# Optimization experiments

Hardware: AMD Instinct MI355X
Metric: run time of the kernel (lower is better)

The kernel has to match this reference:

```python
import jax, jax.numpy as jnp
import numpy as np
from jax import lax

KH, KW, PAD = 3, 3, 1  # kernel_size and paddings from init_kwargs


def _sign_pm1(v):
    # tf.sign with zeros mapped to -1
    return jnp.where(v > 0, jnp.float32(1.0), jnp.float32(-1.0)).astype(v.dtype)


def setup_inputs() -> dict:
    key = jax.random.key(0)
    k1, k2, k3 = jax.random.split(key, 3)
    x = jax.random.normal(k1, (32, 56, 56, 256), dtype=jnp.float32)
    kernel = jax.random.normal(k2, (KH, KW, 256, 256), dtype=jnp.float32) * 0.05
    bias = jax.random.normal(k3, (256,), dtype=jnp.float32) * 0.01
    return {"x": x, "kernel": kernel, "bias": bias}


def reference(x, kernel, bias):
    # pad input spatially (NHWC)
    xp = jnp.pad(x, ((0, 0), (PAD, PAD), (PAD, PAD), (0, 0)))

    # binarize kernel: static batch dim known -> alpha = mean(|W|) over (kh, kw, cin)
    bin_k = _sign_pm1(kernel)
    alpha = jnp.mean(jnp.abs(kernel), axis=(0, 1, 2))  # (Cout,)

    # binarize input: batch dim dynamic in TF -> beta = mean(|x|) over channels, keepdims
    bin_x = _sign_pm1(xp)                               # (N, H+2P, W+2P, C)
    beta = jnp.mean(jnp.abs(xp), axis=3, keepdims=True)  # (N, H+2P, W+2P, 1)

    # K = avg_pool(beta, kernel window, stride 1, VALID)
    K = lax.reduce_window(beta, jnp.float32(0.0), lax.add,
                          (1, KH, KW, 1), (1, 1, 1, 1), 'VALID') / (KH * KW)
    Ka = K * alpha  # (N, H, W, Cout) via broadcast

    conv = lax.conv_general_dilated(
        bin_x, bin_k, window_strides=(1, 1), padding='VALID',
        dimension_numbers=('NHWC', 'HWIO', 'NHWC'))  # (N, H, W, Cout)

    return conv * Ka + bias
```

## Files before the change

kernel.cpp:

```cpp
#include <hip/hip_runtime.h>
#include <cstdint>

#define N_ 32
#define H_ 56
#define W_ 56
#define C_ 256
#define HP 58
#define WP 58


__global__ __launch_bounds__(256) void pack_w(const float* __restrict__ k,
                                              uint64_t* __restrict__ kb,
                                              float* __restrict__ palpha) {
    int idx = blockIdx.x;
    int p = idx >> 2, j = idx & 3;
    int co = threadIdx.x;
    uint64_t bits = 0;
    float s = 0.f;
    #pragma unroll
    for (int b = 0; b < 64; ++b) {
        float v = k[(p * 256 + 4 * b + j) * 256 + co];
        bits |= (uint64_t)(v > 0.f) << b;
        s += fabsf(v);
    }
    kb[((size_t)p * 256 + co) * 4 + j] = bits;
    palpha[idx * 256 + co] = s;
}

__global__ __launch_bounds__(256) void pack_x(const float4* __restrict__ x4,
                                              uint64_t* __restrict__ xb,
                                              float* __restrict__ beta) {
    int bi = blockIdx.x;
    int n = bi / HP, y = bi % HP;
    int wave = threadIdx.x >> 6, lane = threadIdx.x & 63;
    for (int xc = wave; xc < WP; xc += 4) {
        bool inb = (y >= 1 && y <= H_ && xc >= 1 && xc <= W_);
        float4 v = make_float4(0.f, 0.f, 0.f, 0.f);
        if (inb)
            v = x4[(((size_t)n * H_ + (y - 1)) * W_ + (xc - 1)) * 64 + lane];
        uint64_t m0 = __ballot(v.x > 0.f);
        uint64_t m1 = __ballot(v.y > 0.f);
        uint64_t m2 = __ballot(v.z > 0.f);
        uint64_t m3 = __ballot(v.w > 0.f);
        float s = fabsf(v.x) + fabsf(v.y) + fabsf(v.z) + fabsf(v.w);
        #pragma unroll
        for (int m = 32; m >= 1; m >>= 1) s += __shfl_xor(s, m, 64);
        size_t pix = (size_t)bi * WP + xc;
        if (lane < 4) {
            uint64_t mw = (lane == 0) ? m0 : (lane == 1) ? m1 : (lane == 2) ? m2 : m3;
            xb[pix * 4 + lane] = mw;
        }
        if (lane == 0) beta[pix] = s * (1.f / 256.f);
    }
}

__global__ __launch_bounds__(256, 4) void bconv(
        const uint64_t* __restrict__ xb, const float* __restrict__ beta,
        const uint64_t* __restrict__ kb, const float* __restrict__ palpha,
        const float* __restrict__ bias, float* __restrict__ out) {
    int bi = blockIdx.x;
    int n = bi / H_, h = bi % H_;
    int tid = threadIdx.x;
    int half = tid >> 7;
    int col = tid & 127;
    int co = (blockIdx.y << 7) | col;

    __shared__ __align__(16) uint64_t xs[3 * WP * 4];
    __shared__ float brow[3 * WP];
    __shared__ float bS[W_];
    __shared__ uint32_t pb[128 * 15];

    const uint64_t* xsrc = xb + (size_t)(n * HP + h) * WP * 4;
    for (int i = tid; i < 3 * WP * 2; i += 256)
        ((ulonglong2*)xs)[i] = ((const ulonglong2*)xsrc)[i];
    const float* bsrc = beta + (size_t)(n * HP + h) * WP;
    for (int i = tid; i < 3 * WP; i += 256) brow[i] = bsrc[i];
    __syncthreads();

    if (tid < W_) {
        float s = 0.f;
        #pragma unroll
        for (int r = 0; r < 3; ++r)
            #pragma unroll
            for (int d = 0; d < 3; ++d) s += brow[r * WP + tid + d];
        bS[tid] = s * (1.f / 9.f);
    }

    uint64_t kr0[9], kr1[9];
    #pragma unroll
    for (int t = 0; t < 9; ++t) {
        ulonglong2 kp = ((const ulonglong2*)kb)[((size_t)t * 256 + co) * 2 + half];
        kr0[t] = kp.x;
        kr1[t] = kp.y;
    }
    float asum = 0.f;
    #pragma unroll
    for (int i = 0; i < 36; ++i) asum += palpha[i * 256 + co];
    float alpha = asum * (1.f / 2304.f);
    float bv = bias[co];

    for (int chunk = 0; chunk < 4; ++chunk) {
        int w0 = chunk * 14;
        uint32_t acc[14];
        #pragma unroll
        for (int i = 0; i < 14; ++i) acc[i] = 0;

        const uint64_t* base = &xs[w0 * 4 + 2 * half];
        #pragma unroll
        for (int xi = 0; xi < 16; ++xi) {
            #pragma unroll
            for (int r = 0; r < 3; ++r) {
                uint64_t x0 = base[(r * WP + xi) * 4];
                uint64_t x1 = base[(r * WP + xi) * 4 + 1];
                #pragma unroll
                for (int kw = 0; kw < 3; ++kw) {
                    int wl = xi - kw;
                    if (wl >= 0 && wl < 14) {
                        int t = r * 3 + kw;
                        acc[wl] += __popcll(x0 ^ kr0[t]) + __popcll(x1 ^ kr1[t]);
                    }
                }
            }
        }

        __syncthreads();
        if (half == 1) {
            #pragma unroll
            for (int i = 0; i < 14; ++i) pb[col * 15 + i] = acc[i];
        }
        __syncthreads();
        if (half == 0) {
            #pragma unroll
            for (int i = 0; i < 14; ++i) {
                int w = w0 + i;
                int tot = (int)(acc[i] + pb[col * 15 + i]);
                float conv = (float)(2304 - 2 * tot);
                out[((size_t)bi * W_ + w) * C_ + co] = conv * bS[w] * alpha + bv;
            }
        }
    }
}

extern "C" void kernel_launch(void* const* d_in, const int* in_sizes, int n_in,
                              void* d_out, int out_size, void* d_ws, size_t ws_size,
                              hipStream_t stream) {
    const float* x    = (const float*)d_in[0];
    const float* k    = (const float*)d_in[1];
    const float* bias = (const float*)d_in[2];
    float* out = (float*)d_out;

    char* ws = (char*)d_ws;
    uint64_t* kb     = (uint64_t*)(ws);
    float*    palpha = (float*)(ws + 73728);
    uint64_t* xb     = (uint64_t*)(ws + 110592);
    float*    beta   = (float*)(ws + 3555328);

    pack_w<<<36, 256, 0, stream>>>(k, kb, palpha);
    pack_x<<<N_ * HP, 256, 0, stream>>>((const float4*)x, xb, beta);
    bconv<<<dim3(N_ * H_, 2), 256, 0, stream>>>(xb, beta, kb, palpha, bias, out);
}
```

Before: 296.6 us.

## Rewrite binary conv to map output columns to lanes with wave-uniform weights

The convolution kernel is restructured so that each lane owns an input column and loops over 64 output channels per wave. Weight words are read as wave-uniform loads from a new co-major layout, and the three horizontal taps are combined with lane shuffles. Outputs are staged through shared memory for coalesced stores. The weight packing is also split across 1024 threads, alpha gets its own small kernel, and pack_x runs one wave per interior pixel with the padding handled by a memset. The intent is to drop the shared-memory x tile, the two-half reduction and the per-block alpha sums, at the cost of a serial 64-channel loop and extra launches.

New measurement: 427.4 us. 1.44x slower.

```diff
diff --git a/kernel.cpp b/kernel.cpp
--- a/kernel.cpp
+++ b/kernel.cpp
@@ -8,134 +8,130 @@
 #define HP 58
 #define WP 58
 
+#define OFF_KB     0
+#define OFF_PAL    73728
+#define OFF_ALF    110592
+#define OFF_XB     114688
+#define OFF_BETA   3559424
 
-__global__ __launch_bounds__(256) void pack_w(const float* __restrict__ k,
-                                              uint64_t* __restrict__ kb,
-                                              float* __restrict__ palpha) {
-    int idx = blockIdx.x;
-    int p = idx >> 2, j = idx & 3;
-    int co = threadIdx.x;
-    uint64_t bits = 0;
-    float s = 0.f;
+
+__global__ __launch_bounds__(1024) void pack_w(const float* __restrict__ k,
+                                               uint64_t* __restrict__ kb,
+                                               float* __restrict__ palpha) {
+    int p = blockIdx.x >> 2, j = blockIdx.x & 3;
+    int q = threadIdx.x >> 8;
+    int co = threadIdx.x & 255;
+    uint64_t bits = 0; float s = 0.f;
     #pragma unroll
-    for (int b = 0; b < 64; ++b) {
+    for (int i = 0; i < 16; ++i) {
+        int b = q * 16 + i;
         float v = k[(p * 256 + 4 * b + j) * 256 + co];
         bits |= (uint64_t)(v > 0.f) << b;
         s += fabsf(v);
     }
-    kb[((size_t)p * 256 + co) * 4 + j] = bits;
-    palpha[idx * 256 + co] = s;
+    __shared__ uint64_t pb[4][256];
+    __shared__ float ps[4][256];
+    pb[q][co] = bits; ps[q][co] = s;
+    __syncthreads();
+    if (q == 0) {
+        uint64_t w = pb[0][co] | pb[1][co] | pb[2][co] | pb[3][co];
+        float t = ps[0][co] + ps[1][co] + ps[2][co] + ps[3][co];
+        kb[((size_t)co * 9 + p) * 4 + j] = w;
+        palpha[(p * 4 + j) * 256 + co] = t;
+    }
+}
+
+__global__ __launch_bounds__(256) void alpha_k(const float* __restrict__ palpha,
+                                               float* __restrict__ alphaF) {
+    int co = threadIdx.x;
+    float s = 0.f;
+    #pragma unroll
+    for (int i = 0; i < 36; ++i) s += palpha[i * 256 + co];
+    alphaF[co] = s * (1.f / 2304.f);
 }
 
 __global__ __launch_bounds__(256) void pack_x(const float4* __restrict__ x4,
                                               uint64_t* __restrict__ xb,
                                               float* __restrict__ beta) {
-    int bi = blockIdx.x;
-    int n = bi / HP, y = bi % HP;
     int wave = threadIdx.x >> 6, lane = threadIdx.x & 63;
-    for (int xc = wave; xc < WP; xc += 4) {
-        bool inb = (y >= 1 && y <= H_ && xc >= 1 && xc <= W_);
-        float4 v = make_float4(0.f, 0.f, 0.f, 0.f);
-        if (inb)
-            v = x4[(((size_t)n * H_ + (y - 1)) * W_ + (xc - 1)) * 64 + lane];
-        uint64_t m0 = __ballot(v.x > 0.f);
-        uint64_t m1 = __ballot(v.y > 0.f);
-        uint64_t m2 = __ballot(v.z > 0.f);
-        uint64_t m3 = __ballot(v.w > 0.f);
-        float s = fabsf(v.x) + fabsf(v.y) + fabsf(v.z) + fabsf(v.w);
-        #pragma unroll
-        for (int m = 32; m >= 1; m >>= 1) s += __shfl_xor(s, m, 64);
-        size_t pix = (size_t)bi * WP + xc;
-        if (lane < 4) {
-            uint64_t mw = (lane == 0) ? m0 : (lane == 1) ? m1 : (lane == 2) ? m2 : m3;
-            xb[pix * 4 + lane] = mw;
-        }
-        if (lane == 0) beta[pix] = s * (1.f / 256.f);
+    int P = blockIdx.x * 4 + wave;
+    float4 v = x4[(size_t)P * 64 + lane];
+    uint64_t m0 = __ballot(v.x > 0.f);
+    uint64_t m1 = __ballot(v.y > 0.f);
+    uint64_t m2 = __ballot(v.z > 0.f);
+    uint64_t m3 = __ballot(v.w > 0.f);
+    float s = fabsf(v.x) + fabsf(v.y) + fabsf(v.z) + fabsf(v.w);
+    #pragma unroll
+    for (int m = 32; m >= 1; m >>= 1) s += __shfl_xor(s, m, 64);
+    int n = P / (H_ * W_);
+    int r = P % (H_ * W_);
+    int hy = r / W_, wx = r % W_;
+    size_t pp = ((size_t)n * HP + hy + 1) * WP + (wx + 1);
+    if (lane < 4) {
+        uint64_t mw = (lane == 0) ? m0 : (lane == 1) ? m1 : (lane == 2) ? m2 : m3;
+        xb[pp * 4 + lane] = mw;
     }
+    if (lane == 0) beta[pp] = s * (1.f / 256.f);
 }
 
-__global__ __launch_bounds__(256, 4) void bconv(
+__global__ __launch_bounds__(256) void bconv(
         const uint64_t* __restrict__ xb, const float* __restrict__ beta,
-        const uint64_t* __restrict__ kb, const float* __restrict__ palpha,
+        const uint64_t* __restrict__ kb, const float* __restrict__ alphaF,
         const float* __restrict__ bias, float* __restrict__ out) {
-    int bi = blockIdx.x;
-    int n = bi / H_, h = bi % H_;
-    int tid = threadIdx.x;
-    int half = tid >> 7;
-    int col = tid & 127;
-    int co = (blockIdx.y << 7) | col;
+    int bx = blockIdx.x;
+    int n = bx / H_, h = bx % H_;
+    int wave = threadIdx.x >> 6, lane = threadIdx.x & 63;
+    int co0 = wave * 64;
+    int c = lane < 57 ? lane : 57;
 
-    __shared__ __align__(16) uint64_t xs[3 * WP * 4];
-    __shared__ float brow[3 * WP];
-    __shared__ float bS[W_];
-    __shared__ uint32_t pb[128 * 15];
+    uint64_t xw[3][4];
+    #pragma unroll
+    for (int r = 0; r < 3; ++r) {
+        const ulonglong2* p2 =
+            (const ulonglong2*)(xb + ((size_t)(n * HP + h + r) * WP + c) * 4);
+        ulonglong2 a = p2[0], b = p2[1];
+        xw[r][0] = a.x; xw[r][1] = a.y; xw[r][2] = b.x; xw[r][3] = b.y;
+    }
 
-    const uint64_t* xsrc = xb + (size_t)(n * HP + h) * WP * 4;
-    for (int i = tid; i < 3 * WP * 2; i += 256)
-        ((ulonglong2*)xs)[i] = ((const ulonglong2*)xsrc)[i];
-    const float* bsrc = beta + (size_t)(n * HP + h) * WP;
-    for (int i = tid; i < 3 * WP; i += 256) brow[i] = bsrc[i];
-    __syncthreads();
-
-    if (tid < W_) {
-        float s = 0.f;
+    float bSw = 0.f;
+    if (lane < W_) {
         #pragma unroll
         for (int r = 0; r < 3; ++r)
             #pragma unroll
-            for (int d = 0; d < 3; ++d) s += brow[r * WP + tid + d];
-        bS[tid] = s * (1.f / 9.f);
+            for (int d = 0; d < 3; ++d)
+                bSw += beta[(size_t)(n * HP + h + r) * WP + lane + d];
+        bSw *= (1.f / 9.f);
     }
 
-    uint64_t kr0[9], kr1[9];
-    #pragma unroll
-    for (int t = 0; t < 9; ++t) {
-        ulonglong2 kp = ((const ulonglong2*)kb)[((size_t)t * 256 + co) * 2 + half];
-        kr0[t] = kp.x;
-        kr1[t] = kp.y;
-    }
-    float asum = 0.f;
-    #pragma unroll
-    for (int i = 0; i < 36; ++i) asum += palpha[i * 256 + co];
-    float alpha = asum * (1.f / 2304.f);
-    float bv = bias[co];
+    __shared__ float ts[4][W_ * 17];
+    float* t = ts[wave];
+    float* orow = out + (size_t)bx * W_ * C_;
 
-    for (int chunk = 0; chunk < 4; ++chunk) {
-        int w0 = chunk * 14;
-        uint32_t acc[14];
+    for (int ci = 0; ci < 64; ++ci) {
+        int co = co0 + ci;
+        const uint64_t* kr = kb + (size_t)co * 36;
+        uint32_t T0 = 0, T1 = 0, T2 = 0;
         #pragma unroll
-        for (int i = 0; i < 14; ++i) acc[i] = 0;
-
-        const uint64_t* base = &xs[w0 * 4 + 2 * half];
-        #pragma unroll
-        for (int xi = 0; xi < 16; ++xi) {
+        for (int r = 0; r < 3; ++r) {
             #pragma unroll
-            for (int r = 0; r < 3; ++r) {
-                uint64_t x0 = base[(r * WP + xi) * 4];
-                uint64_t x1 = base[(r * WP + xi) * 4 + 1];
-                #pragma unroll
-                for (int kw = 0; kw < 3; ++kw) {
-                    int wl = xi - kw;
-                    if (wl >= 0 && wl < 14) {
-                        int t = r * 3 + kw;
-                        acc[wl] += __popcll(x0 ^ kr0[t]) + __popcll(x1 ^ kr1[t]);
-                    }
-                }
+            for (int j = 0; j < 4; ++j) {
+                uint64_t xv = xw[r][j];
+                T0 += __popcll(xv ^ kr[(r * 3 + 0) * 4 + j]);
+                T1 += __popcll(xv ^ kr[(r * 3 + 1) * 4 + j]);
+                T2 += __popcll(xv ^ kr[(r * 3 + 2) * 4 + j]);
             }
         }
-
-        __syncthreads();
-        if (half == 1) {
-            #pragma unroll
-            for (int i = 0; i < 14; ++i) pb[col * 15 + i] = acc[i];
-        }
-        __syncthreads();
-        if (half == 0) {
+        uint32_t tot = T0 + __shfl_down(T1, 1) + __shfl_down(T2, 2);
+        float conv = (float)(2304 - 2 * (int)tot);
+        float res = conv * bSw * alphaF[co] + bias[co];
+        if (lane < W_) t[lane * 17 + (ci & 15)] = res;
+        if ((ci & 15) == 15) {
+            int cb = co0 + (ci & ~15);
             #pragma unroll
             for (int i = 0; i < 14; ++i) {
-                int w = w0 + i;
-                int tot = (int)(acc[i] + pb[col * 15 + i]);
-                float conv = (float)(2304 - 2 * tot);
-                out[((size_t)bi * W_ + w) * C_ + co] = conv * bS[w] * alpha + bv;
+                int idx = i * 64 + lane;
+                int w = idx >> 4, cc = idx & 15;
+                orow[(size_t)w * C_ + cb + cc] = t[w * 17 + cc];
             }
         }
     }
@@ -150,12 +146,16 @@
     float* out = (float*)d_out;
 
     char* ws = (char*)d_ws;
-    uint64_t* kb     = (uint64_t*)(ws);
-    float*    palpha = (float*)(ws + 73728);
-    uint64_t* xb     = (uint64_t*)(ws + 110592);
-    float*    beta   = (float*)(ws + 3555328);
+    uint64_t* kb     = (uint64_t*)(ws + OFF_KB);
+    float*    palpha = (float*)(ws + OFF_PAL);
+    float*    alphaF = (float*)(ws + OFF_ALF);
+    uint64_t* xb     = (uint64_t*)(ws + OFF_XB);
+    float*    beta   = (float*)(ws + OFF_BETA);
 
-    pack_w<<<36, 256, 0, stream>>>(k, kb, palpha);
-    pack_x<<<N_ * HP, 256, 0, stream>>>((const float4*)x, xb, beta);
-    bconv<<<dim3(N_ * H_, 2), 256, 0, stream>>>(xb, beta, kb, palpha, bias, out);
+    hipMemsetAsync(ws + OFF_XB, 0, 3444736 + 430592, stream);
+
+    pack_w<<<36, 1024, 0, stream>>>(k, kb, palpha);
+    alpha_k<<<1, 256, 0, stream>>>(palpha, alphaF);
+    pack_x<<<(N_ * H_ * W_) / 4, 256, 0, stream>>>((const float4*)x, xb, beta);
+    bconv<<<N_ * H_, 256, 0, stream>>>(xb, beta, kb, alphaF, bias, out);
 }
```
